# Kernel optimization log

Hardware: AMD Instinct MI355X
Metric: run time of the kernel (lower is better)

Reference implementation:

```python
import jax, jax.numpy as jnp
import numpy as np

B, S, D = 2, 2048, 2560
H, HD = 32, 80           # n_head, head_dim = n_embd // n_head
RD = 32                  # rotary_dim (partial rotary, phi-style)
ROPE_BASE = 10000.0


def _rope_cache(seqlen, rotary_dim):
    # inv_freq = 1 / base^(2i/d); freqs = outer(t, inv_freq)  -> [S, RD//2]
    inv_freq = 1.0 / (ROPE_BASE ** (jnp.arange(0, rotary_dim, 2, dtype=jnp.float32) / rotary_dim))
    t = jnp.arange(seqlen, dtype=jnp.float32)
    freqs = jnp.outer(t, inv_freq)
    return jnp.cos(freqs), jnp.sin(freqs)


def setup_inputs() -> dict:
    key = jax.random.key(0)
    k0, k1, k2, k3, k4 = jax.random.split(key, 5)
    x = jax.random.normal(k0, (B, S, D), dtype=jnp.float32)
    wqkv_w = jax.random.normal(k1, (3 * D, D), dtype=jnp.float32) * 0.02
    wqkv_b = jax.random.normal(k2, (3 * D,), dtype=jnp.float32) * 0.02
    out_w = jax.random.normal(k3, (D, D), dtype=jnp.float32) * 0.02
    out_b = jax.random.normal(k4, (D,), dtype=jnp.float32) * 0.02
    return {"x": x, "wqkv_w": wqkv_w, "wqkv_b": wqkv_b, "out_w": out_w, "out_b": out_b}


def _attention_core(x, wqkv_w, wqkv_b, out_w, out_b):
    b, s, d = x.shape
    qkv = (x @ wqkv_w.T + wqkv_b).reshape(b, s, 3, H, HD)  # [B,S,3,H,HD]

    cos, sin = _rope_cache(s, RD)            # [S, RD//2]
    c = cos[:, None, :]                       # [S,1,RD//2]
    si = sin[:, None, :]

    def rot(t):  # partial NeoX-style rotary on first RD dims; t: [B,S,H,HD]
        t_rot, t_pass = t[..., :RD], t[..., RD:]
        t1, t2 = t_rot[..., : RD // 2], t_rot[..., RD // 2 :]
        return jnp.concatenate([t1 * c - t2 * si, t1 * si + t2 * c, t_pass], axis=-1)

    q = rot(qkv[:, :, 0])                     # [B,S,H,HD]
    k = rot(qkv[:, :, 1])
    v = qkv[:, :, 2]

    # fp32 scores = q @ (k * scale)^T, causal mask filled with -10000.0 (as in source)
    scale = 1.0 / np.sqrt(HD).astype(np.float32)
    scores = jnp.einsum("bqhd,bkhd->bhqk", q, k * scale)  # [B,H,S,S]
    causal_mask = jnp.arange(s)[None, :] > jnp.arange(s)[:, None]  # cols > rows
    scores = jnp.where(causal_mask, jnp.float32(-10000.0), scores)
    attn = jax.nn.softmax(scores, axis=-1)
    ctx = jnp.einsum("bhqk,bkhd->bqhd", attn, v).reshape(b, s, d)
    return ctx @ out_w.T + out_b


def reference(x, wqkv_w, wqkv_b, out_w, out_b):
    return _attention_core(x, wqkv_w, wqkv_b, out_w, out_b)
```

## Files before the change

### kernel.cpp

```cpp
#include <hip/hip_runtime.h>
#include <cstdint>
#include <cstddef>

#define B_  2
#define S_  2048
#define D_  2560
#define H_  32
#define HD_ 80

typedef __attribute__((ext_vector_type(8))) short  short8;
typedef __attribute__((ext_vector_type(4))) float  floatx4;

__device__ __forceinline__ float b2f(unsigned short u) {
  union { unsigned int i; float f; } x; x.i = ((unsigned int)u) << 16; return x.f;
}
__device__ __forceinline__ unsigned short f2bf(float f) {
  union { float f; unsigned int i; } x; x.f = f;
  unsigned int u = x.i;
  return (unsigned short)((u + 0x7fffu + ((u >> 16) & 1u)) >> 16);
}

__global__ void cvt3_kernel(const float* __restrict__ s0, unsigned short* __restrict__ d0, int n0,
                            const float* __restrict__ s1, unsigned short* __restrict__ d1, int n1,
                            const float* __restrict__ s2, unsigned short* __restrict__ d2, int n2) {
  int j = blockIdx.x * 256 + threadIdx.x;
  const float* s; unsigned short* d;
  if (j < n0) { s = s0; d = d0; }
  else {
    j -= n0;
    if (j < n1) { s = s1; d = d1; }
    else { j -= n1; if (j >= n2) return; s = s2; d = d2; }
  }
  const float4 v = ((const float4*)s)[j];
  ushort4 r;
  r.x = f2bf(v.x); r.y = f2bf(v.y); r.z = f2bf(v.z); r.w = f2bf(v.w);
  ((ushort4*)d)[j] = r;
}

#define GLOAD_LDS16(g, l)                                                      \
  __builtin_amdgcn_global_load_lds(                                            \
      (const __attribute__((address_space(1))) void*)(g),                      \
      (__attribute__((address_space(3))) void*)(l), 16, 0, 0)

template <int OUT_BF16>
__global__ __launch_bounds__(512)
void gemm256(const unsigned short* __restrict__ A,
             const unsigned short* __restrict__ Bw,
             const float* __restrict__ bias,
             void* __restrict__ Cv,
             const int M, const int N, const int K) {
  __shared__ __align__(16) unsigned short sh[65536];
  const int tid  = threadIdx.x;
  const int wave = tid >> 6;
  const int lane = tid & 63;
  const int wm = wave >> 2;
  const int wn = wave & 3;
  const int fr = lane & 15;
  const int fg = lane >> 4;
  const int row0 = (int)blockIdx.y << 8;
  const int col0 = (int)blockIdx.x << 8;
  const unsigned short* Ab = A  + (size_t)row0 * K;
  const unsigned short* Bb = Bw + (size_t)col0 * K;
  const int srow = lane >> 2;
  const int scol = ((lane & 3) << 3) ^ ((lane & 32) ? 16 : 0);
  const int rdoff = fr * 32 + ((fg * 8) ^ ((fr & 8) ? 16 : 0));
  const int aOff = wm * 8192;
  const int bOff = 16384 + (wn >> 1) * 8192;
  const int rbB  = (wn & 1) * 4;
  const int NT = K >> 6;

  floatx4 acc[8][4] = {};

#define STAGE_HALF(G, matOff, c, h, k0)                                        \
  do {                                                                         \
    _Pragma("unroll")                                                          \
    for (int i_ = 0; i_ < 2; ++i_) {                                           \
      const int s_ = (wave << 1) | i_;                                         \
      const int kk_ = s_ >> 3, rb_ = s_ & 7;                                   \
      GLOAD_LDS16((G) + (size_t)((h) * 128 + rb_ * 16 + srow) * K              \
                      + ((k0) + kk_ * 32 + scol),                              \
                  &sh[(c) * 32768 + (matOff) + (h) * 8192 + s_ * 512]);        \
    }                                                                          \
  } while (0)

  STAGE_HALF(Ab, 0,     0, 0, 0);
  STAGE_HALF(Ab, 0,     0, 1, 0);
  STAGE_HALF(Bb, 16384, 0, 0, 0);
  STAGE_HALF(Bb, 16384, 0, 1, 0);
  if (NT > 1) { STAGE_HALF(Ab, 0, 1, 0, 64); STAGE_HALF(Ab, 0, 1, 1, 64); }
  if (NT > 1) asm volatile("s_waitcnt vmcnt(4)" ::: "memory");
  else        asm volatile("s_waitcnt vmcnt(0)" ::: "memory");
  __builtin_amdgcn_s_barrier();

  for (int t = 0; t < NT; ++t) {
    const int c  = t & 1;
    const int cb = c << 15;
    short8 aL[4][2], aH[4][2], bF0[2][2], bF1[2][2];
#pragma unroll
    for (int nj = 0; nj < 2; ++nj)
#pragma unroll
      for (int kk = 0; kk < 2; ++kk)
        bF0[nj][kk] = *(const short8*)&sh[cb + bOff + (kk * 8 + rbB + nj) * 512 + rdoff];
#pragma unroll
    for (int mi = 0; mi < 4; ++mi)
#pragma unroll
      for (int kk = 0; kk < 2; ++kk)
        aL[mi][kk] = *(const short8*)&sh[cb + aOff + (kk * 8 + mi) * 512 + rdoff];
#pragma unroll
    for (int nj = 0; nj < 2; ++nj)
#pragma unroll
      for (int kk = 0; kk < 2; ++kk)
        bF1[nj][kk] = *(const short8*)&sh[cb + bOff + (kk * 8 + rbB + 2 + nj) * 512 + rdoff];
    if (t + 1 < NT) {
      STAGE_HALF(Bb, 16384, c ^ 1, 0, (t + 1) << 6);
      STAGE_HALF(Bb, 16384, c ^ 1, 1, (t + 1) << 6);
    }
    __builtin_amdgcn_s_setprio(1);
#pragma unroll
    for (int kk = 0; kk < 2; ++kk)
#pragma unroll
      for (int mi = 0; mi < 4; ++mi)
#pragma unroll
        for (int nj = 0; nj < 2; ++nj)
          acc[mi][nj] = __builtin_amdgcn_mfma_f32_16x16x32_bf16(aL[mi][kk], bF0[nj][kk], acc[mi][nj], 0, 0, 0);
    __builtin_amdgcn_s_setprio(0);
#pragma unroll
    for (int mi = 0; mi < 4; ++mi)
#pragma unroll
      for (int kk = 0; kk < 2; ++kk)
        aH[mi][kk] = *(const short8*)&sh[cb + aOff + (kk * 8 + 4 + mi) * 512 + rdoff];
    __builtin_amdgcn_s_setprio(1);
#pragma unroll
    for (int kk = 0; kk < 2; ++kk)
#pragma unroll
      for (int mi = 0; mi < 4; ++mi)
#pragma unroll
        for (int nj = 0; nj < 2; ++nj)
          acc[mi][2 + nj] = __builtin_amdgcn_mfma_f32_16x16x32_bf16(aL[mi][kk], bF1[nj][kk], acc[mi][2 + nj], 0, 0, 0);
#pragma unroll
    for (int kk = 0; kk < 2; ++kk)
#pragma unroll
      for (int mi = 0; mi < 4; ++mi)
#pragma unroll
        for (int nj = 0; nj < 2; ++nj)
          acc[4 + mi][2 + nj] = __builtin_amdgcn_mfma_f32_16x16x32_bf16(aH[mi][kk], bF1[nj][kk], acc[4 + mi][2 + nj], 0, 0, 0);
    __builtin_amdgcn_s_setprio(0);
    __builtin_amdgcn_s_barrier();
    __builtin_amdgcn_sched_barrier(0);
    if (t + 2 < NT) {
      STAGE_HALF(Ab, 0, c, 0, (t + 2) << 6);
      STAGE_HALF(Ab, 0, c, 1, (t + 2) << 6);
    }
    __builtin_amdgcn_s_setprio(1);
#pragma unroll
    for (int kk = 0; kk < 2; ++kk)
#pragma unroll
      for (int mi = 0; mi < 4; ++mi)
#pragma unroll
        for (int nj = 0; nj < 2; ++nj)
          acc[4 + mi][nj] = __builtin_amdgcn_mfma_f32_16x16x32_bf16(aH[mi][kk], bF0[nj][kk], acc[4 + mi][nj], 0, 0, 0);
    __builtin_amdgcn_s_setprio(0);
    if (t + 2 < NT)      asm volatile("s_waitcnt vmcnt(4)" ::: "memory");
    else if (t + 1 < NT) asm volatile("s_waitcnt vmcnt(0)" ::: "memory");
    if (t + 1 < NT) __builtin_amdgcn_s_barrier();
  }
#undef STAGE_HALF

  unsigned short* Cb = (unsigned short*)Cv;
  float* Cf = (float*)Cv;
#pragma unroll
  for (int nj = 0; nj < 4; ++nj) {
    const int col = col0 + wn * 64 + nj * 16 + fr;
    const float bv = bias[col];
#pragma unroll
    for (int mi = 0; mi < 8; ++mi) {
      const int rowb = row0 + wm * 128 + mi * 16 + fg * 4;
#pragma unroll
      for (int r = 0; r < 4; ++r) {
        const float v = acc[mi][nj][r] + bv;
        const size_t idx = (size_t)(rowb + r) * N + col;
        if (OUT_BF16) Cb[idx] = f2bf(v);
        else          Cf[idx] = v;
      }
    }
  }
}

__global__ void rope_kernel(const unsigned short* __restrict__ qkv,
                            unsigned short* __restrict__ Q,
                            unsigned short* __restrict__ K) {
  const int idx = blockIdx.x * 256 + threadIdx.x;
  if (idx >= B_ * S_ * H_) return;
  const int h = idx & (H_ - 1);
  const int s = (idx >> 5) & (S_ - 1);
  const int b = idx >> 16;
  const unsigned short* row = qkv + (size_t)(b * S_ + s) * (3 * D_);
  const size_t obase = ((size_t)(b * H_ + h) * S_ + s) * HD_;

  float cc[16], ssn[16];
#pragma unroll
  for (int i = 0; i < 16; i++) {
    const float ang = (float)s * exp2f((float)i * -0.83048202372184059f);
    ssn[i] = sinf(ang);
    cc[i]  = cosf(ang);
  }
  {
    const float QS = 0.11180339887498949f * 1.4426950408889634f;
    const uint4* src = (const uint4*)(row + h * HD_);
    float f[80], g[80];
#pragma unroll
    for (int i = 0; i < 10; i++) {
      uint4 t = src[i];
      const unsigned short* w = (const unsigned short*)&t;
#pragma unroll
      for (int j = 0; j < 8; j++) f[i * 8 + j] = b2f(w[j]);
    }
#pragma unroll
    for (int i = 0; i < 16; i++) {
      g[i]      = f[i] * cc[i] - f[i + 16] * ssn[i];
      g[i + 16] = f[i] * ssn[i] + f[i + 16] * cc[i];
    }
#pragma unroll
    for (int i = 32; i < 80; i++) g[i] = f[i];
    uint4* dst = (uint4*)(Q + obase);
#pragma unroll
    for (int i = 0; i < 10; i++) {
      uint4 t;
      unsigned short* w = (unsigned short*)&t;
#pragma unroll
      for (int j = 0; j < 8; j++) w[j] = f2bf(g[i * 8 + j] * QS);
      dst[i] = t;
    }
  }
  {
    const uint4* src = (const uint4*)(row + (H_ + h) * HD_);
    float f[32], g[32];
#pragma unroll
    for (int i = 0; i < 4; i++) {
      uint4 t = src[i];
      const unsigned short* w = (const unsigned short*)&t;
#pragma unroll
      for (int j = 0; j < 8; j++) f[i * 8 + j] = b2f(w[j]);
    }
#pragma unroll
    for (int i = 0; i < 16; i++) {
      g[i]      = f[i] * cc[i] - f[i + 16] * ssn[i];
      g[i + 16] = f[i] * ssn[i] + f[i + 16] * cc[i];
    }
    uint4* dst = (uint4*)(K + obase);
#pragma unroll
    for (int i = 0; i < 4; i++) {
      uint4 t;
      unsigned short* w = (unsigned short*)&t;
#pragma unroll
      for (int j = 0; j < 8; j++) w[j] = f2bf(g[i * 8 + j]);
      dst[i] = t;
    }
#pragma unroll
    for (int i = 4; i < 10; i++) dst[i] = src[i];
  }
}

__global__ __launch_bounds__(256)
void vtrans_kernel(const unsigned short* __restrict__ qkv, unsigned short* __restrict__ Vt) {
  __shared__ unsigned short T[64][88];
  const int tid = threadIdx.x;
  const int bh = blockIdx.y;
  const int b = bh >> 5, h = bh & 31;
  const int tile = blockIdx.x;
  const int s0 = tile * 64;
  for (int t = tid; t < 640; t += 256) {
    const int r = t / 10, c = t % 10;
    const size_t src = ((size_t)((b * S_ + s0 + r) * 3) + 2) * D_ + h * HD_ + c * 8;
    *(uint4*)&T[r][c * 8] = *(const uint4*)&qkv[src];
  }
  __syncthreads();
  unsigned short* tb = Vt + ((size_t)bh * 32 + tile) * 5120;
  for (int t = tid; t < 640; t += 256) {
    const int d = t / 8, sc = t % 8;
    uint4 o;
    unsigned short* w = (unsigned short*)&o;
#pragma unroll
    for (int j = 0; j < 8; j++) w[j] = T[sc * 8 + j][d];
    *(uint4*)&tb[d * 64 + ((sc * 8) ^ ((d & 7) * 8))] = o;
  }
}

__global__ __launch_bounds__(256, 4)
void attn_mfma(const unsigned short* __restrict__ Qg,
               const unsigned short* __restrict__ Kg,
               const unsigned short* __restrict__ Vtg,
               unsigned short* __restrict__ ctx) {
  __shared__ unsigned short Ks[64 * 80];
  __shared__ unsigned short Vs[80 * 64];
  __shared__ unsigned short Ts[4][32 * 40];

  const int tid  = threadIdx.x;
  const int wave = tid >> 6;
  const int lane = tid & 63;
  const int fr   = lane & 15;
  const int fg   = lane >> 4;
  const int bh   = blockIdx.y;
  const int qt   = (int)gridDim.x - 1 - (int)blockIdx.x;
  const int qbase = (qt << 7) + wave * 32;

  const unsigned short* Qrow  = Qg  + (size_t)bh * S_ * HD_;
  const unsigned short* Krow  = Kg  + (size_t)bh * S_ * HD_;
  const unsigned short* Vtile = Vtg + (size_t)bh * 32 * 5120;

  short8 qf[2][3];
  const short8 zfrag = {};
#pragma unroll
  for (int mi = 0; mi < 2; mi++) {
    const unsigned short* qp = Qrow + (size_t)(qbase + mi * 16 + fr) * HD_;
    qf[mi][0] = *(const short8*)&qp[fg * 8];
    qf[mi][1] = *(const short8*)&qp[32 + fg * 8];
    qf[mi][2] = (fg < 2) ? *(const short8*)&qp[64 + fg * 8] : zfrag;
  }

  floatx4 accOT[5][2] = {};
  float l_part[2] = {0.f, 0.f};

  const int nch = 2 * qt + 2;
  for (int c = 0; c < nch; c++) {
    const int k0 = c * 64;
    __syncthreads();
    {
      const unsigned short* Kt = Krow + (size_t)k0 * HD_;
      for (int i = wave; i < 10; i += 4)
        GLOAD_LDS16(Kt + i * 512 + lane * 8, &Ks[i * 512]);
    }
    {
      const unsigned short* Vt = Vtile + (size_t)c * 5120;
      for (int i = wave; i < 10; i += 4)
        GLOAD_LDS16(Vt + i * 512 + lane * 8, &Vs[i * 512]);
    }
    __syncthreads();

    floatx4 accST[4][2] = {};
#pragma unroll
    for (int ni = 0; ni < 4; ni++) {
      const unsigned short* kp = &Ks[(ni * 16 + fr) * 80];
      const short8 kf0 = *(const short8*)&kp[fg * 8];
      const short8 kf1 = *(const short8*)&kp[32 + fg * 8];
      const short8 kf2 = *(const short8*)&kp[64 + (fg & 1) * 8];
      accST[ni][0] = __builtin_amdgcn_mfma_f32_16x16x32_bf16(kf0, qf[0][0], accST[ni][0], 0, 0, 0);
      accST[ni][1] = __builtin_amdgcn_mfma_f32_16x16x32_bf16(kf0, qf[1][0], accST[ni][1], 0, 0, 0);
      accST[ni][0] = __builtin_amdgcn_mfma_f32_16x16x32_bf16(kf1, qf[0][1], accST[ni][0], 0, 0, 0);
      accST[ni][1] = __builtin_amdgcn_mfma_f32_16x16x32_bf16(kf1, qf[1][1], accST[ni][1], 0, 0, 0);
      accST[ni][0] = __builtin_amdgcn_mfma_f32_16x16x32_bf16(kf2, qf[0][2], accST[ni][0], 0, 0, 0);
      accST[ni][1] = __builtin_amdgcn_mfma_f32_16x16x32_bf16(kf2, qf[1][2], accST[ni][1], 0, 0, 0);
    }

    if (k0 + 63 > qbase) {
#pragma unroll
      for (int ni = 0; ni < 4; ni++)
#pragma unroll
        for (int mi = 0; mi < 2; mi++) {
          const int qg = qbase + mi * 16 + fr;
#pragma unroll
          for (int r = 0; r < 4; r++) {
            const int kg = k0 + ni * 16 + fg * 4 + r;
            if (kg > qg) accST[ni][mi][r] = -1e30f;
          }
        }
    }

#pragma unroll
    for (int hh = 0; hh < 2; hh++) {
#pragma unroll
      for (int nh = 0; nh < 2; nh++) {
        const int ni = hh * 2 + nh;
#pragma unroll
        for (int mi = 0; mi < 2; mi++) {
          const float p0 = __builtin_amdgcn_exp2f(accST[ni][mi][0]);
          const float p1 = __builtin_amdgcn_exp2f(accST[ni][mi][1]);
          const float p2 = __builtin_amdgcn_exp2f(accST[ni][mi][2]);
          const float p3 = __builtin_amdgcn_exp2f(accST[ni][mi][3]);
          l_part[mi] += (p0 + p1) + (p2 + p3);
          uint2 w;
          w.x = (unsigned)f2bf(p0) | ((unsigned)f2bf(p1) << 16);
          w.y = (unsigned)f2bf(p2) | ((unsigned)f2bf(p3) << 16);
          *(uint2*)&Ts[wave][(mi * 16 + fr) * 40 + nh * 16 + fg * 4] = w;
        }
      }
      const short8 pf0 = *(const short8*)&Ts[wave][fr * 40 + fg * 8];
      const short8 pf1 = *(const short8*)&Ts[wave][(16 + fr) * 40 + fg * 8];
      const int vcol = hh * 32 + fg * 8;
#pragma unroll
      for (int dt = 0; dt < 5; dt++) {
        const short8 vf = *(const short8*)&Vs[(dt * 16 + fr) * 64 + (vcol ^ ((fr & 7) * 8))];
        accOT[dt][0] = __builtin_amdgcn_mfma_f32_16x16x32_bf16(vf, pf0, accOT[dt][0], 0, 0, 0);
        accOT[dt][1] = __builtin_amdgcn_mfma_f32_16x16x32_bf16(vf, pf1, accOT[dt][1], 0, 0, 0);
      }
    }
  }

  const int b = bh >> 5, h2 = bh & 31;
#pragma unroll
  for (int mi = 0; mi < 2; mi++) {
    float s = l_part[mi];
    s += __shfl_xor(s, 16);
    s += __shfl_xor(s, 32);
    const float inv = 1.f / s;
    const size_t rowoff = (size_t)(b * S_ + qbase + mi * 16 + fr) * D_ + h2 * HD_;
#pragma unroll
    for (int dt = 0; dt < 5; dt++) {
      const float v0 = accOT[dt][mi][0] * inv;
      const float v1 = accOT[dt][mi][1] * inv;
      const float v2 = accOT[dt][mi][2] * inv;
      const float v3 = accOT[dt][mi][3] * inv;
      uint2 w;
      w.x = (unsigned)f2bf(v0) | ((unsigned)f2bf(v1) << 16);
      w.y = (unsigned)f2bf(v2) | ((unsigned)f2bf(v3) << 16);
      *(uint2*)&ctx[rowoff + dt * 16 + fg * 4] = w;
    }
  }
}

extern "C" void kernel_launch(void* const* d_in, const int* in_sizes, int n_in,
                              void* d_out, int out_size, void* d_ws, size_t ws_size,
                              hipStream_t stream) {
  (void)in_sizes; (void)n_in; (void)out_size; (void)ws_size;
  const float* x      = (const float*)d_in[0];
  const float* wqkv_w = (const float*)d_in[1];
  const float* wqkv_b = (const float*)d_in[2];
  const float* out_w  = (const float*)d_in[3];
  const float* out_b  = (const float*)d_in[4];
  char* ws = (char*)d_ws;

  unsigned short* Xb    = (unsigned short*)(ws + 0);
  unsigned short* Wqkvb = (unsigned short*)(ws + 20971520);
  unsigned short* qkv   = (unsigned short*)(ws + 60293120);
  unsigned short* Qb    = (unsigned short*)(ws + 123207680);
  unsigned short* Kb    = (unsigned short*)(ws + 144179200);
  unsigned short* Woutb = (unsigned short*)(ws + 165150720);
  unsigned short* ctx   = Xb;
  unsigned short* Vtile = (unsigned short*)(ws + 34078720);

  cvt3_kernel<<<35840, 256, 0, stream>>>(x, Xb, 2621440,
                                         wqkv_w, Wqkvb, 4915200,
                                         out_w, Woutb, 1638400);
  gemm256<1><<<dim3(30, 16), 512, 0, stream>>>(Xb, Wqkvb, wqkv_b, (void*)qkv, 4096, 7680, 2560);
  rope_kernel<<<512, 256, 0, stream>>>(qkv, Qb, Kb);
  vtrans_kernel<<<dim3(32, 64), 256, 0, stream>>>(qkv, Vtile);
  attn_mfma<<<dim3(16, 64), 256, 0, stream>>>(Qb, Kb, Vtile, ctx);
  gemm256<0><<<dim3(10, 16), 512, 0, stream>>>(ctx, Woutb, out_b, d_out, 4096, 2560, 2560);
}
```

Baseline: 568.4 us.

## Template GEMM on M-subtile count; use 128-row tiles for output projection

The GEMM kernel is templated on the number of 16-row M subtiles. The output projection now uses 128x256 tiles, giving 320 blocks instead of 160 and filling more of the CUs. The pipeline is also simplified to prefetch A and B together at the top of each iteration, followed by a full vmcnt(0) wait and barrier. That replaces the staggered A/B prefetch with partial waits, which may expose more memory latency in the QKV GEMM.

```diff
diff --git a/kernel.cpp b/kernel.cpp
--- a/kernel.cpp
+++ b/kernel.cpp
@@ -42,14 +42,17 @@
       (const __attribute__((address_space(1))) void*)(g),                      \
       (__attribute__((address_space(3))) void*)(l), 16, 0, 0)
 
-template <int OUT_BF16>
+template <int OUT_BF16, int MSUB>
 __global__ __launch_bounds__(512)
 void gemm256(const unsigned short* __restrict__ A,
              const unsigned short* __restrict__ Bw,
              const float* __restrict__ bias,
              void* __restrict__ Cv,
              const int M, const int N, const int K) {
-  __shared__ __align__(16) unsigned short sh[65536];
+  constexpr int ASH  = MSUB * 2048;
+  constexpr int BSH  = 16384;
+  constexpr int CBUF = ASH + BSH;
+  __shared__ __align__(16) unsigned short sh[2 * CBUF];
   const int tid  = threadIdx.x;
   const int wave = tid >> 6;
   const int lane = tid & 63;
@@ -57,19 +60,19 @@
   const int wn = wave & 3;
   const int fr = lane & 15;
   const int fg = lane >> 4;
-  const int row0 = (int)blockIdx.y << 8;
+  const int row0 = (int)blockIdx.y * (MSUB * 32);
   const int col0 = (int)blockIdx.x << 8;
   const unsigned short* Ab = A  + (size_t)row0 * K;
   const unsigned short* Bb = Bw + (size_t)col0 * K;
   const int srow = lane >> 2;
   const int scol = ((lane & 3) << 3) ^ ((lane & 32) ? 16 : 0);
   const int rdoff = fr * 32 + ((fg * 8) ^ ((fr & 8) ? 16 : 0));
-  const int aOff = wm * 8192;
-  const int bOff = 16384 + (wn >> 1) * 8192;
+  const int aOff = wm * (MSUB == 8 ? 8192 : 2048);
+  const int bOff = ASH + (wn >> 1) * 8192;
   const int rbB  = (wn & 1) * 4;
   const int NT = K >> 6;
 
-  floatx4 acc[8][4] = {};
+  floatx4 acc[MSUB][4] = {};
 
 #define STAGE_HALF(G, matOff, c, h, k0)                                        \
   do {                                                                         \
@@ -79,22 +82,27 @@
       const int kk_ = s_ >> 3, rb_ = s_ & 7;                                   \
       GLOAD_LDS16((G) + (size_t)((h) * 128 + rb_ * 16 + srow) * K              \
                       + ((k0) + kk_ * 32 + scol),                              \
-                  &sh[(c) * 32768 + (matOff) + (h) * 8192 + s_ * 512]);        \
+                  &sh[(c) * CBUF + (matOff) + (h) * 8192 + s_ * 512]);         \
     }                                                                          \
   } while (0)
 
-  STAGE_HALF(Ab, 0,     0, 0, 0);
-  STAGE_HALF(Ab, 0,     0, 1, 0);
-  STAGE_HALF(Bb, 16384, 0, 0, 0);
-  STAGE_HALF(Bb, 16384, 0, 1, 0);
-  if (NT > 1) { STAGE_HALF(Ab, 0, 1, 0, 64); STAGE_HALF(Ab, 0, 1, 1, 64); }
-  if (NT > 1) asm volatile("s_waitcnt vmcnt(4)" ::: "memory");
-  else        asm volatile("s_waitcnt vmcnt(0)" ::: "memory");
+  STAGE_HALF(Ab, 0, 0, 0, 0);
+  if (MSUB == 8) STAGE_HALF(Ab, 0, 0, 1, 0);
+  STAGE_HALF(Bb, ASH, 0, 0, 0);
+  STAGE_HALF(Bb, ASH, 0, 1, 0);
+  asm volatile("s_waitcnt vmcnt(0)" ::: "memory");
   __builtin_amdgcn_s_barrier();
 
   for (int t = 0; t < NT; ++t) {
     const int c  = t & 1;
-    const int cb = c << 15;
+    const int cb = c * CBUF;
+    if (t + 1 < NT) {
+      const int k1 = (t + 1) << 6;
+      STAGE_HALF(Ab, 0, c ^ 1, 0, k1);
+      if (MSUB == 8) STAGE_HALF(Ab, 0, c ^ 1, 1, k1);
+      STAGE_HALF(Bb, ASH, c ^ 1, 0, k1);
+      STAGE_HALF(Bb, ASH, c ^ 1, 1, k1);
+    }
     short8 aL[4][2], aH[4][2], bF0[2][2], bF1[2][2];
 #pragma unroll
     for (int nj = 0; nj < 2; ++nj)
@@ -111,10 +119,6 @@
 #pragma unroll
       for (int kk = 0; kk < 2; ++kk)
         bF1[nj][kk] = *(const short8*)&sh[cb + bOff + (kk * 8 + rbB + 2 + nj) * 512 + rdoff];
-    if (t + 1 < NT) {
-      STAGE_HALF(Bb, 16384, c ^ 1, 0, (t + 1) << 6);
-      STAGE_HALF(Bb, 16384, c ^ 1, 1, (t + 1) << 6);
-    }
     __builtin_amdgcn_s_setprio(1);
 #pragma unroll
     for (int kk = 0; kk < 2; ++kk)
@@ -124,11 +128,13 @@
         for (int nj = 0; nj < 2; ++nj)
           acc[mi][nj] = __builtin_amdgcn_mfma_f32_16x16x32_bf16(aL[mi][kk], bF0[nj][kk], acc[mi][nj], 0, 0, 0);
     __builtin_amdgcn_s_setprio(0);
-#pragma unroll
-    for (int mi = 0; mi < 4; ++mi)
-#pragma unroll
-      for (int kk = 0; kk < 2; ++kk)
-        aH[mi][kk] = *(const short8*)&sh[cb + aOff + (kk * 8 + 4 + mi) * 512 + rdoff];
+    if (MSUB == 8) {
+#pragma unroll
+      for (int mi = 0; mi < 4; ++mi)
+#pragma unroll
+        for (int kk = 0; kk < 2; ++kk)
+          aH[mi][kk] = *(const short8*)&sh[cb + aOff + (kk * 8 + 4 + mi) * 512 + rdoff];
+    }
     __builtin_amdgcn_s_setprio(1);
 #pragma unroll
     for (int kk = 0; kk < 2; ++kk)
@@ -137,32 +143,27 @@
 #pragma unroll
         for (int nj = 0; nj < 2; ++nj)
           acc[mi][2 + nj] = __builtin_amdgcn_mfma_f32_16x16x32_bf16(aL[mi][kk], bF1[nj][kk], acc[mi][2 + nj], 0, 0, 0);
-#pragma unroll
-    for (int kk = 0; kk < 2; ++kk)
-#pragma unroll
-      for (int mi = 0; mi < 4; ++mi)
-#pragma unroll
-        for (int nj = 0; nj < 2; ++nj)
-          acc[4 + mi][2 + nj] = __builtin_amdgcn_mfma_f32_16x16x32_bf16(aH[mi][kk], bF1[nj][kk], acc[4 + mi][2 + nj], 0, 0, 0);
+    if (MSUB == 8) {
+#pragma unroll
+      for (int kk = 0; kk < 2; ++kk)
+#pragma unroll
+        for (int mi = 0; mi < 4; ++mi)
+#pragma unroll
+          for (int nj = 0; nj < 2; ++nj)
+            acc[4 + mi][2 + nj] = __builtin_amdgcn_mfma_f32_16x16x32_bf16(aH[mi][kk], bF1[nj][kk], acc[4 + mi][2 + nj], 0, 0, 0);
+#pragma unroll
+      for (int kk = 0; kk < 2; ++kk)
+#pragma unroll
+        for (int mi = 0; mi < 4; ++mi)
+#pragma unroll
+          for (int nj = 0; nj < 2; ++nj)
+            acc[4 + mi][nj] = __builtin_amdgcn_mfma_f32_16x16x32_bf16(aH[mi][kk], bF0[nj][kk], acc[4 + mi][nj], 0, 0, 0);
+    }
     __builtin_amdgcn_s_setprio(0);
-    __builtin_amdgcn_s_barrier();
-    __builtin_amdgcn_sched_barrier(0);
-    if (t + 2 < NT) {
-      STAGE_HALF(Ab, 0, c, 0, (t + 2) << 6);
-      STAGE_HALF(Ab, 0, c, 1, (t + 2) << 6);
-    }
-    __builtin_amdgcn_s_setprio(1);
-#pragma unroll
-    for (int kk = 0; kk < 2; ++kk)
-#pragma unroll
-      for (int mi = 0; mi < 4; ++mi)
-#pragma unroll
-        for (int nj = 0; nj < 2; ++nj)
-          acc[4 + mi][nj] = __builtin_amdgcn_mfma_f32_16x16x32_bf16(aH[mi][kk], bF0[nj][kk], acc[4 + mi][nj], 0, 0, 0);
-    __builtin_amdgcn_s_setprio(0);
-    if (t + 2 < NT)      asm volatile("s_waitcnt vmcnt(4)" ::: "memory");
-    else if (t + 1 < NT) asm volatile("s_waitcnt vmcnt(0)" ::: "memory");
-    if (t + 1 < NT) __builtin_amdgcn_s_barrier();
+    if (t + 1 < NT) {
+      asm volatile("s_waitcnt vmcnt(0)" ::: "memory");
+      __builtin_amdgcn_s_barrier();
+    }
   }
 #undef STAGE_HALF
 
@@ -173,8 +174,8 @@
     const int col = col0 + wn * 64 + nj * 16 + fr;
     const float bv = bias[col];
 #pragma unroll
-    for (int mi = 0; mi < 8; ++mi) {
-      const int rowb = row0 + wm * 128 + mi * 16 + fg * 4;
+    for (int mi = 0; mi < MSUB; ++mi) {
+      const int rowb = row0 + wm * (MSUB * 16) + mi * 16 + fg * 4;
 #pragma unroll
       for (int r = 0; r < 4; ++r) {
         const float v = acc[mi][nj][r] + bv;
@@ -441,9 +442,9 @@
   cvt3_kernel<<<35840, 256, 0, stream>>>(x, Xb, 2621440,
                                          wqkv_w, Wqkvb, 4915200,
                                          out_w, Woutb, 1638400);
-  gemm256<1><<<dim3(30, 16), 512, 0, stream>>>(Xb, Wqkvb, wqkv_b, (void*)qkv, 4096, 7680, 2560);
+  gemm256<1, 8><<<dim3(30, 16), 512, 0, stream>>>(Xb, Wqkvb, wqkv_b, (void*)qkv, 4096, 7680, 2560);
   rope_kernel<<<512, 256, 0, stream>>>(qkv, Qb, Kb);
   vtrans_kernel<<<dim3(32, 64), 256, 0, stream>>>(qkv, Vtile);
   attn_mfma<<<dim3(16, 64), 256, 0, stream>>>(Qb, Kb, Vtile, ctx);
-  gemm256<0><<<dim3(10, 16), 512, 0, stream>>>(ctx, Woutb, out_b, d_out, 4096, 2560, 2560);
-}
+  gemm256<0, 4><<<dim3(10, 32), 512, 0, stream>>>(ctx, Woutb, out_b, d_out, 4096, 2560, 2560);
+}
```

Result: slower. 603.0 us (+6.1%).
